# Optimization experiments

Hardware: AMD Instinct MI355X
Metric: run time of the kernel (lower is better)

Reference implementation:

```python
import jax, jax.numpy as jnp
import numpy as np

H = 8          # num_heads
D = 64         # out_dim per head
ROT = D // 2   # rotary dim per spatial axis (out_dim // relative_emb_dim)
MIN_FREQ = 1.0 / 64


def _freqs(t):
    # t: (bs, N) coordinates -> (bs, N, ROT)
    inv_freq = 1.0 / (10000.0 ** (jnp.arange(0, ROT, 2, dtype=jnp.float32) / ROT))
    f = (t / MIN_FREQ)[..., None] * inv_freq  # (bs, N, ROT/2)
    return jnp.concatenate([f, f], axis=-1)   # (bs, N, ROT)


def _rotate_half(x):
    x1, x2 = jnp.split(x, 2, axis=-1)
    return jnp.concatenate([-x2, x1], axis=-1)


def _rope(t, f):
    return t * jnp.cos(f) + _rotate_half(t) * jnp.sin(f)


def reference(h, pos, Wq, Wk, Wv, src, dst):
    bs, N, _ = pos.shape
    hb = h.reshape(bs, N, -1)                       # (bs, N, C)
    # Faithful to torch: Linear output (bs,N,H*D) .view(bs,H,N,D) is a raw
    # memory reinterpretation, i.e. a reshape, not a transpose.
    Qh = (hb @ Wq.T).reshape(bs, H, N, D)
    Kh = (hb @ Wk.T).reshape(bs, H, N, D)
    Vh = (hb @ Wv.T).reshape(bs, H, N, D)

    fx = _freqs(pos[..., 0])[:, None]               # (bs, 1, N, ROT) broadcast over heads
    fy = _freqs(pos[..., 1])[:, None]

    def rope2d(t):
        return jnp.concatenate([_rope(t[..., :ROT], fx), _rope(t[..., ROT:], fy)], axis=-1)

    Qh = rope2d(Qh)
    Kh = rope2d(Kh)

    Qn = Qh.reshape(-1, H, D)                       # (bs*N, H, D) flat node layout
    Kn = Kh.reshape(-1, H, D)
    Vn = Vh.reshape(-1, H, D)

    # edge attention: gather, dot, clamped exp, scatter-sum
    score = jnp.sum(Kn[src] * Qn[dst], axis=-1)     # (E, H)
    score = jnp.exp(jnp.clip(score / np.sqrt(D).astype(np.float32), -5.0, 5.0))

    nseg = bs * N
    wV = jax.ops.segment_sum(Vn[src] * score[..., None], dst, num_segments=nseg)  # (nseg,H,D)
    z = jax.ops.segment_sum(score, dst, num_segments=nseg)                        # (nseg,H)

    attn_out = wV / z[..., None]
    return attn_out.reshape(-1, H * D)


def setup_inputs() -> dict:
    key = jax.random.key(0)
    k = jax.random.split(key, 7)
    bs, N, C, E = 4, 4096, 256, 524288
    return {
        "h": jax.random.normal(k[0], (bs * N, C), dtype=jnp.float32),
        "pos": jax.random.uniform(k[1], (bs, N, 2), dtype=jnp.float32),
        "Wq": jax.random.normal(k[2], (H * D, C), dtype=jnp.float32) * 0.05,
        "Wk": jax.random.normal(k[3], (H * D, C), dtype=jnp.float32) * 0.05,
        "Wv": jax.random.normal(k[4], (H * D, C), dtype=jnp.float32) * 0.05,
        "src": jax.random.randint(k[5], (E,), 0, bs * N, dtype=jnp.int32),
        "dst": jax.random.randint(k[6], (E,), 0, bs * N, dtype=jnp.int32),
    }
```

## Files before the change

kernel.cpp:

```cpp
#include <hip/hip_runtime.h>
#include <math.h>

#define NODES 16384
#define CIN   256
#define HD    512
#define NPOS  4096
#define NHEAD 8
#define DDIM  64
#define HN    (NODES * CIN)
#define WN    (HD * CIN)

typedef float f32x4 __attribute__((ext_vector_type(4)));
typedef unsigned int u32x4 __attribute__((ext_vector_type(4)));
typedef short s16x8 __attribute__((ext_vector_type(8)));

__device__ inline unsigned short f2bf(float f) {
  unsigned int u = __float_as_uint(f);
  u += 0x7fffu + ((u >> 16) & 1u);
  return (unsigned short)(u >> 16);
}

__global__ __launch_bounds__(256) void conv_kernel(
    const float* __restrict__ h, const float* __restrict__ wq,
    const float* __restrict__ wk, const float* __restrict__ wv,
    unsigned short* __restrict__ out) {
  size_t e = ((size_t)blockIdx.x * 256 + threadIdx.x) * 8;
  const float* s;
  size_t off;
  if (e < HN)               { s = h;  off = e; }
  else if (e < HN + WN)     { s = wq; off = e - HN; }
  else if (e < HN + 2 * WN) { s = wk; off = e - HN - WN; }
  else                      { s = wv; off = e - HN - 2 * WN; }
  float4 f0 = *(const float4*)(s + off);
  float4 f1 = *(const float4*)(s + off + 4);
  u32x4 o;
  o[0] = f2bf(f0.x) | ((unsigned int)f2bf(f0.y) << 16);
  o[1] = f2bf(f0.z) | ((unsigned int)f2bf(f0.w) << 16);
  o[2] = f2bf(f1.x) | ((unsigned int)f2bf(f1.y) << 16);
  o[3] = f2bf(f1.z) | ((unsigned int)f2bf(f1.w) << 16);
  *(u32x4*)(out + e) = o;
}

__global__ __launch_bounds__(256) void gemm_mfma_kernel(
    const unsigned short* __restrict__ hb,
    const unsigned short* __restrict__ wb,
    unsigned short* __restrict__ Qb, unsigned short* __restrict__ Kb,
    unsigned short* __restrict__ Vb) {
  const unsigned short* B = wb + (size_t)blockIdx.z * WN;
  unsigned short* C = blockIdx.z == 0 ? Qb : (blockIdx.z == 1 ? Kb : Vb);

  __shared__ __align__(16) unsigned short As[128 * 32];
  __shared__ __align__(16) unsigned short Bs[128 * 32];

  const int tid = threadIdx.x;
  const int lane = tid & 63, w = tid >> 6;
  const int row0 = blockIdx.y * 128, col0 = blockIdx.x * 128;
  const int wr = w >> 1, wc = w & 1;

  f32x4 acc[4][4] = {};

  for (int kt = 0; kt < CIN; kt += 32) {
#pragma unroll
    for (int u = 0; u < 2; ++u) {
      int blk = u * 4 + w;
      int r = blk * 16 + (lane >> 2);
      int kc = (lane & 3) * 8;
      __builtin_amdgcn_global_load_lds(
          (const __attribute__((address_space(1))) void*)(hb + (size_t)(row0 + r) * CIN + kt + kc),
          (__attribute__((address_space(3))) void*)(As + blk * 512), 16, 0, 0);
      __builtin_amdgcn_global_load_lds(
          (const __attribute__((address_space(1))) void*)(B + (size_t)(col0 + r) * CIN + kt + kc),
          (__attribute__((address_space(3))) void*)(Bs + blk * 512), 16, 0, 0);
    }
    __syncthreads();

    s16x8 af[4], bfr[4];
#pragma unroll
    for (int mi = 0; mi < 4; ++mi)
      af[mi] = *(const s16x8*)(As + (wr * 64 + mi * 16 + (lane & 15)) * 32 + (lane >> 4) * 8);
#pragma unroll
    for (int ni = 0; ni < 4; ++ni)
      bfr[ni] = *(const s16x8*)(Bs + (wc * 64 + ni * 16 + (lane & 15)) * 32 + (lane >> 4) * 8);
#pragma unroll
    for (int mi = 0; mi < 4; ++mi)
#pragma unroll
      for (int ni = 0; ni < 4; ++ni)
        acc[mi][ni] = __builtin_amdgcn_mfma_f32_16x16x32_bf16(
            af[mi], bfr[ni], acc[mi][ni], 0, 0, 0);
    __syncthreads();
  }

#pragma unroll
  for (int mi = 0; mi < 4; ++mi) {
    int rbase = row0 + wr * 64 + mi * 16 + (lane >> 4) * 4;
#pragma unroll
    for (int ni = 0; ni < 4; ++ni) {
      int c = col0 + wc * 64 + ni * 16 + (lane & 15);
#pragma unroll
      for (int r = 0; r < 4; ++r)
        C[(size_t)(rbase + r) * HD + c] = f2bf(acc[mi][ni][r]);
    }
  }
}

__global__ __launch_bounds__(256) void rope_kernel(
    unsigned short* __restrict__ Qb, unsigned short* __restrict__ Kb,
    const float* __restrict__ pos) {
  const float INVF[16] = {
      1.0f, 0.5623413252f, 0.3162277660f, 0.1778279410f,
      0.1f, 0.05623413252f, 0.03162277660f, 0.01778279410f,
      0.01f, 0.005623413252f, 0.003162277660f, 0.001778279410f,
      0.001f, 0.0005623413252f, 0.0003162277660f, 0.0001778279410f};
  int t = blockIdx.x * 256 + threadIdx.x;
  unsigned short* M = (t >> 18) ? Kb : Qb;
  int p = t & ((1 << 18) - 1);
  int rem = p >> 1, q = p & 1;
  int n = rem & (NPOS - 1);
  int b = rem >> 15;
  float ps = pos[((size_t)((b << 12) + n)) * 2 + q] * 64.0f;

  unsigned short* base = M + (size_t)rem * DDIM + q * 32;
  u32x4 lo0 = *(u32x4*)(base);
  u32x4 lo1 = *(u32x4*)(base + 8);
  u32x4 hi0 = *(u32x4*)(base + 16);
  u32x4 hi1 = *(u32x4*)(base + 24);
  float lo[16], hi[16];
#pragma unroll
  for (int j = 0; j < 4; ++j) {
    lo[2 * j]     = __uint_as_float(lo0[j] << 16);
    lo[2 * j + 1] = __uint_as_float(lo0[j] & 0xffff0000u);
    lo[8 + 2 * j]     = __uint_as_float(lo1[j] << 16);
    lo[8 + 2 * j + 1] = __uint_as_float(lo1[j] & 0xffff0000u);
    hi[2 * j]     = __uint_as_float(hi0[j] << 16);
    hi[2 * j + 1] = __uint_as_float(hi0[j] & 0xffff0000u);
    hi[8 + 2 * j]     = __uint_as_float(hi1[j] << 16);
    hi[8 + 2 * j + 1] = __uint_as_float(hi1[j] & 0xffff0000u);
  }
  unsigned short o[32];
#pragma unroll
  for (int i = 0; i < 16; ++i) {
    float s, c;
    sincosf(ps * INVF[i], &s, &c);
    o[i]      = f2bf(lo[i] * c - hi[i] * s);
    o[i + 16] = f2bf(hi[i] * c + lo[i] * s);
  }
  u32x4 ov;
#pragma unroll
  for (int blkk = 0; blkk < 4; ++blkk) {
#pragma unroll
    for (int j = 0; j < 4; ++j)
      ov[j] = (unsigned int)o[blkk * 8 + 2 * j] |
              ((unsigned int)o[blkk * 8 + 2 * j + 1] << 16);
    *(u32x4*)(base + blkk * 8) = ov;
  }
}

__global__ __launch_bounds__(256) void hist_kernel(
    const int* __restrict__ dst, int* __restrict__ count, int E) {
  int t = blockIdx.x * 256 + threadIdx.x;
  if (t < E) atomicAdd(&count[dst[t]], 1);
}

__global__ __launch_bounds__(256) void scan_kernel(
    const int* __restrict__ count, int* __restrict__ offset,
    int* __restrict__ cursor) {
  __shared__ int psum[256];
  __shared__ int pref[256];
  int t = threadIdx.x;
  int base = t * (NODES / 256);
  int s = 0;
  for (int i = 0; i < NODES / 256; ++i) s += count[base + i];
  psum[t] = s;
  __syncthreads();
  if (t == 0) {
    int run = 0;
    for (int i = 0; i < 256; ++i) { pref[i] = run; run += psum[i]; }
  }
  __syncthreads();
  int off = pref[t];
  for (int i = 0; i < NODES / 256; ++i) {
    int c = count[base + i];
    offset[base + i] = off;
    cursor[base + i] = off;
    off += c;
  }
  if (t == 255) offset[NODES] = off;
}

__global__ __launch_bounds__(256) void scatter_kernel(
    const int* __restrict__ src, const int* __restrict__ dst,
    int* __restrict__ cursor, int* __restrict__ srcs, int E) {
  int t = blockIdx.x * 256 + threadIdx.x;
  if (t < E) {
    int p = atomicAdd(&cursor[dst[t]], 1);
    srcs[p] = src[t];
  }
}

__global__ __launch_bounds__(256) void node_kernel(
    const unsigned short* __restrict__ Qb, const unsigned short* __restrict__ Kb,
    const unsigned short* __restrict__ Vb,
    const int* __restrict__ srcs, const int* __restrict__ offset,
    float* __restrict__ out) {
  __shared__ float wv[4][HD];
  __shared__ float zb[4][NHEAD];
  const int n = blockIdx.x;
  const int tid = threadIdx.x;
  const int lane = tid & 63, w = tid >> 6;
  const int hh = lane >> 3, g = lane & 7;

  const int beg = offset[n], end = offset[n + 1];

  u32x4 qu = *(const u32x4*)(Qb + (size_t)n * HD + lane * 8);
  float qf[8];
#pragma unroll
  for (int j = 0; j < 4; ++j) {
    qf[2 * j]     = __uint_as_float(qu[j] << 16);
    qf[2 * j + 1] = __uint_as_float(qu[j] & 0xffff0000u);
  }

  float a[8] = {0, 0, 0, 0, 0, 0, 0, 0};
  float zacc = 0.f;

  for (int i = beg + w; i < end; i += 4) {
    int s = srcs[i];
    u32x4 ku = *(const u32x4*)(Kb + (size_t)s * HD + lane * 8);
    float dot = 0.f;
#pragma unroll
    for (int j = 0; j < 4; ++j) {
      dot += __uint_as_float(ku[j] << 16) * qf[2 * j];
      dot += __uint_as_float(ku[j] & 0xffff0000u) * qf[2 * j + 1];
    }
    dot += __shfl_xor(dot, 1);
    dot += __shfl_xor(dot, 2);
    dot += __shfl_xor(dot, 4);
    float sc = expf(fminf(fmaxf(dot * 0.125f, -5.0f), 5.0f));
    u32x4 vu = *(const u32x4*)(Vb + (size_t)s * HD + lane * 8);
#pragma unroll
    for (int j = 0; j < 4; ++j) {
      a[2 * j]     += __uint_as_float(vu[j] << 16) * sc;
      a[2 * j + 1] += __uint_as_float(vu[j] & 0xffff0000u) * sc;
    }
    zacc += sc;
  }

  *(float4*)&wv[w][lane * 8]     = make_float4(a[0], a[1], a[2], a[3]);
  *(float4*)&wv[w][lane * 8 + 4] = make_float4(a[4], a[5], a[6], a[7]);
  if (g == 0) zb[w][hh] = zacc;
  __syncthreads();

  const int d0 = tid * 2;
  float r0 = wv[0][d0] + wv[1][d0] + wv[2][d0] + wv[3][d0];
  float r1 = wv[0][d0 + 1] + wv[1][d0 + 1] + wv[2][d0 + 1] + wv[3][d0 + 1];
  const int head = d0 >> 6;
  float zz = zb[0][head] + zb[1][head] + zb[2][head] + zb[3][head];
  float inv = 1.0f / zz;
  *(float2*)&out[(size_t)n * HD + d0] = make_float2(r0 * inv, r1 * inv);
}

extern "C" void kernel_launch(void* const* d_in, const int* in_sizes, int n_in,
                              void* d_out, int out_size, void* d_ws,
                              size_t ws_size, hipStream_t stream) {
  const float* h   = (const float*)d_in[0];
  const float* pos = (const float*)d_in[1];
  const float* Wq  = (const float*)d_in[2];
  const float* Wk  = (const float*)d_in[3];
  const float* Wv  = (const float*)d_in[4];
  const int* src   = (const int*)d_in[5];
  const int* dst   = (const int*)d_in[6];
  const int E = in_sizes[5];

  unsigned short* hb  = (unsigned short*)d_ws;
  unsigned short* wb  = hb + HN;
  unsigned short* Qb  = wb + 3 * WN;
  unsigned short* Kb  = Qb + (size_t)NODES * HD;
  unsigned short* Vb  = Kb + (size_t)NODES * HD;
  int* count  = (int*)(Vb + (size_t)NODES * HD);
  int* offset = count + NODES;
  int* cursor = offset + NODES + 1;
  int* srcs   = cursor + NODES;
  float* out = (float*)d_out;

  hipMemsetAsync(count, 0, NODES * sizeof(int), stream);

  conv_kernel<<<(HN + 3 * WN) / 8 / 256, 256, 0, stream>>>(h, Wq, Wk, Wv, hb);

  gemm_mfma_kernel<<<dim3(HD / 128, NODES / 128, 3), 256, 0, stream>>>(
      hb, wb, Qb, Kb, Vb);

  rope_kernel<<<(2 * 131072 * 2) / 256, 256, 0, stream>>>(Qb, Kb, pos);

  hist_kernel<<<(E + 255) / 256, 256, 0, stream>>>(dst, count, E);
  scan_kernel<<<1, 256, 0, stream>>>(count, offset, cursor);
  scatter_kernel<<<(E + 255) / 256, 256, 0, stream>>>(src, dst, cursor, srcs, E);

  node_kernel<<<NODES, 256, 0, stream>>>(Qb, Kb, Vb, srcs, offset, out);
}
```

Before: 322.0 us.

## Double-buffer GEMM LDS tiles and unroll edge gather loop by two

The projection GEMM now double-buffers its shared-memory tiles, prefetching the next K slice with async global-to-LDS loads while MFMAs run on the current one. The edge attention loop processes two edges per wave per iteration and issues K and V gathers up front, so more random loads are in flight at once. The cost is twice the LDS per GEMM block and more registers in the attention kernel, which may lower occupancy. There is also a possible hazard: the prefetch is issued without an explicit wait for the async LDS loads before the next read, so correctness relies on the barrier draining them.

```diff
diff --git a/kernel.cpp b/kernel.cpp
--- a/kernel.cpp
+++ b/kernel.cpp
@@ -49,46 +49,62 @@
   const unsigned short* B = wb + (size_t)blockIdx.z * WN;
   unsigned short* C = blockIdx.z == 0 ? Qb : (blockIdx.z == 1 ? Kb : Vb);
 
-  __shared__ __align__(16) unsigned short As[128 * 32];
-  __shared__ __align__(16) unsigned short Bs[128 * 32];
+  __shared__ __align__(16) unsigned short As[2][128 * 32];
+  __shared__ __align__(16) unsigned short Bs[2][128 * 32];
 
   const int tid = threadIdx.x;
   const int lane = tid & 63, w = tid >> 6;
   const int row0 = blockIdx.y * 128, col0 = blockIdx.x * 128;
   const int wr = w >> 1, wc = w & 1;
 
+  const int r_l = lane >> 2;
+  const int kc = (lane & 3) * 8;
+
   f32x4 acc[4][4] = {};
 
-  for (int kt = 0; kt < CIN; kt += 32) {
-#pragma unroll
-    for (int u = 0; u < 2; ++u) {
-      int blk = u * 4 + w;
-      int r = blk * 16 + (lane >> 2);
-      int kc = (lane & 3) * 8;
-      __builtin_amdgcn_global_load_lds(
-          (const __attribute__((address_space(1))) void*)(hb + (size_t)(row0 + r) * CIN + kt + kc),
-          (__attribute__((address_space(3))) void*)(As + blk * 512), 16, 0, 0);
-      __builtin_amdgcn_global_load_lds(
-          (const __attribute__((address_space(1))) void*)(B + (size_t)(col0 + r) * CIN + kt + kc),
-          (__attribute__((address_space(3))) void*)(Bs + blk * 512), 16, 0, 0);
-    }
-    __syncthreads();
+#define STAGE(bufi, kt)                                                        \
+  {                                                                            \
+    _Pragma("unroll") for (int u = 0; u < 2; ++u) {                            \
+      int blk = u * 4 + w;                                                     \
+      int r = blk * 16 + r_l;                                                  \
+      __builtin_amdgcn_global_load_lds(                                        \
+          (const __attribute__((address_space(1))) void*)(hb +                 \
+              (size_t)(row0 + r) * CIN + (kt) + kc),                           \
+          (__attribute__((address_space(3))) void*)(&As[bufi][blk * 512]),     \
+          16, 0, 0);                                                           \
+      __builtin_amdgcn_global_load_lds(                                        \
+          (const __attribute__((address_space(1))) void*)(B +                  \
+              (size_t)(col0 + r) * CIN + (kt) + kc),                           \
+          (__attribute__((address_space(3))) void*)(&Bs[bufi][blk * 512]),     \
+          16, 0, 0);                                                           \
+    }                                                                          \
+  }
+
+  STAGE(0, 0);
+  __syncthreads();
+
+  int cur = 0;
+  for (int t = 0; t < 8; ++t) {
+    if (t < 7) STAGE(cur ^ 1, (t + 1) * 32);
 
     s16x8 af[4], bfr[4];
 #pragma unroll
     for (int mi = 0; mi < 4; ++mi)
-      af[mi] = *(const s16x8*)(As + (wr * 64 + mi * 16 + (lane & 15)) * 32 + (lane >> 4) * 8);
+      af[mi] = *(const s16x8*)(&As[cur][(wr * 64 + mi * 16 + (lane & 15)) * 32 + (lane >> 4) * 8]);
 #pragma unroll
     for (int ni = 0; ni < 4; ++ni)
-      bfr[ni] = *(const s16x8*)(Bs + (wc * 64 + ni * 16 + (lane & 15)) * 32 + (lane >> 4) * 8);
+      bfr[ni] = *(const s16x8*)(&Bs[cur][(wc * 64 + ni * 16 + (lane & 15)) * 32 + (lane >> 4) * 8]);
 #pragma unroll
     for (int mi = 0; mi < 4; ++mi)
 #pragma unroll
       for (int ni = 0; ni < 4; ++ni)
         acc[mi][ni] = __builtin_amdgcn_mfma_f32_16x16x32_bf16(
             af[mi], bfr[ni], acc[mi][ni], 0, 0, 0);
+
     __syncthreads();
-  }
+    cur ^= 1;
+  }
+#undef STAGE
 
 #pragma unroll
   for (int mi = 0; mi < 4; ++mi) {
@@ -222,9 +238,43 @@
   float a[8] = {0, 0, 0, 0, 0, 0, 0, 0};
   float zacc = 0.f;
 
-  for (int i = beg + w; i < end; i += 4) {
+  int i = beg + w;
+  for (; i + 4 < end; i += 8) {
+    int s0 = srcs[i];
+    int s1 = srcs[i + 4];
+    u32x4 ku0 = *(const u32x4*)(Kb + (size_t)s0 * HD + lane * 8);
+    u32x4 ku1 = *(const u32x4*)(Kb + (size_t)s1 * HD + lane * 8);
+    u32x4 vu0 = *(const u32x4*)(Vb + (size_t)s0 * HD + lane * 8);
+    u32x4 vu1 = *(const u32x4*)(Vb + (size_t)s1 * HD + lane * 8);
+    float dot0 = 0.f, dot1 = 0.f;
+#pragma unroll
+    for (int j = 0; j < 4; ++j) {
+      dot0 += __uint_as_float(ku0[j] << 16) * qf[2 * j];
+      dot0 += __uint_as_float(ku0[j] & 0xffff0000u) * qf[2 * j + 1];
+      dot1 += __uint_as_float(ku1[j] << 16) * qf[2 * j];
+      dot1 += __uint_as_float(ku1[j] & 0xffff0000u) * qf[2 * j + 1];
+    }
+    dot0 += __shfl_xor(dot0, 1);
+    dot1 += __shfl_xor(dot1, 1);
+    dot0 += __shfl_xor(dot0, 2);
+    dot1 += __shfl_xor(dot1, 2);
+    dot0 += __shfl_xor(dot0, 4);
+    dot1 += __shfl_xor(dot1, 4);
+    float sc0 = expf(fminf(fmaxf(dot0 * 0.125f, -5.0f), 5.0f));
+    float sc1 = expf(fminf(fmaxf(dot1 * 0.125f, -5.0f), 5.0f));
+#pragma unroll
+    for (int j = 0; j < 4; ++j) {
+      a[2 * j]     += __uint_as_float(vu0[j] << 16) * sc0 +
+                      __uint_as_float(vu1[j] << 16) * sc1;
+      a[2 * j + 1] += __uint_as_float(vu0[j] & 0xffff0000u) * sc0 +
+                      __uint_as_float(vu1[j] & 0xffff0000u) * sc1;
+    }
+    zacc += sc0 + sc1;
+  }
+  for (; i < end; i += 4) {
     int s = srcs[i];
     u32x4 ku = *(const u32x4*)(Kb + (size_t)s * HD + lane * 8);
+    u32x4 vu = *(const u32x4*)(Vb + (size_t)s * HD + lane * 8);
     float dot = 0.f;
 #pragma unroll
     for (int j = 0; j < 4; ++j) {
@@ -235,7 +285,6 @@
     dot += __shfl_xor(dot, 2);
     dot += __shfl_xor(dot, 4);
     float sc = expf(fminf(fmaxf(dot * 0.125f, -5.0f), 5.0f));
-    u32x4 vu = *(const u32x4*)(Vb + (size_t)s * HD + lane * 8);
 #pragma unroll
     for (int j = 0; j < 4; ++j) {
       a[2 * j]     += __uint_as_float(vu[j] << 16) * sc;
```

New measurement: 320.4 us. No clear change (-0.5%).
